# Optimization experiments

Hardware: AMD Instinct MI355X
Metric: run time of the kernel (lower is better)

The kernel has to match this reference:

```python
import jax, jax.numpy as jnp
import numpy as np


def setup_inputs() -> dict:
    key = jax.random.key(0)
    k1, k2, k3 = jax.random.split(key, 3)
    B, L, D = 2, 8192, 1024
    x = jax.random.normal(k1, (B, L, D), dtype=jnp.float32)
    h = jax.random.normal(k2, (L, D), dtype=jnp.float32)
    bias = jax.random.normal(k3, (D,), dtype=jnp.float32) * 0.02
    return {"x": x, "h": h, "bias": bias}


def reference(x, h, bias):
    # x: (B, L, D), h: (filter_len, D), bias: (D,)
    B, L, D = x.shape
    filter_len = h.shape[0]
    # next power of two >= L + filter_len - 1 (static, from shapes)
    fft_size = 1 << int(L + filter_len - 1).bit_length()
    x_f = jnp.fft.rfft(x, n=fft_size, axis=1)          # (B, fft_size//2+1, D) complex
    h_f = jnp.fft.rfft(h, n=fft_size, axis=0)          # (fft_size//2+1, D) complex
    y = jnp.fft.irfft(x_f * h_f[None, :, :], n=fft_size, axis=1)
    y = y[:, :L, :]                                    # causal-length truncation
    return y + bias
```

## Files before the change

### kernel.cpp

```cpp
#include <hip/hip_runtime.h>

#define D_CH   1024
#define L_SEQ  8192
#define TWO_PI 6.28318530717958647692f
#define W_N    3.8349519697141029e-4f
#define W128A  4.90873852123405e-2f

__device__ __forceinline__ unsigned f2bf(float v){
  union { float f; unsigned u; } x; x.f = v;
  unsigned r = x.u + 0x7fffu + ((x.u >> 16) & 1u);
  return r >> 16;
}
__device__ __forceinline__ float bf2f(unsigned v){
  union { float f; unsigned u; } x; x.u = v << 16;
  return x.f;
}
__device__ __forceinline__ unsigned packc(float r, float i){
  return f2bf(r) | (f2bf(i) << 16);
}
__device__ __forceinline__ float2 upk(unsigned u){
  return make_float2(bf2f(u & 0xffffu), bf2f(u >> 16));
}

__device__ __host__ constexpr int bitrev4(int j){
  return ((j&1)<<3)|((j&2)<<1)|((j&4)>>1)|((j&8)>>3);
}
__device__ __host__ constexpr int bitrev3(int j){
  return ((j&1)<<2)|(j&2)|((j&4)>>2);
}

template<int SGN>
__device__ __forceinline__ void dft16(float2* x){
  const float TC[8] = {1.f, 0.9238795325f, 0.7071067812f, 0.3826834324f,
                       0.f, -0.3826834324f, -0.7071067812f, -0.9238795325f};
  const float TS[8] = {0.f, -0.3826834324f, -0.7071067812f, -0.9238795325f,
                       -1.f, -0.9238795325f, -0.7071067812f, -0.3826834324f};
#pragma unroll
  for (int len = 16; len >= 2; len >>= 1){
    const int half = len >> 1, tstep = 16 / len;
#pragma unroll
    for (int st = 0; st < 16; st += len){
#pragma unroll
      for (int j = 0; j < half; j++){
        const float wr = TC[j*tstep];
        const float wi = (SGN > 0) ? TS[j*tstep] : -TS[j*tstep];
        const int a = st + j, b = a + half;
        const float ur = x[a].x, ui = x[a].y;
        const float vr = x[b].x, vi = x[b].y;
        x[a].x = ur + vr; x[a].y = ui + vi;
        const float dr = ur - vr, di = ui - vi;
        x[b].x = dr*wr - di*wi;
        x[b].y = dr*wi + di*wr;
      }
    }
  }
}

template<int SGN>
__device__ __forceinline__ void dft8(float2* x){
  const float TC[4] = {1.f, 0.7071067812f, 0.f, -0.7071067812f};
  const float TS[4] = {0.f, -0.7071067812f, -1.f, -0.7071067812f};
#pragma unroll
  for (int len = 8; len >= 2; len >>= 1){
    const int half = len >> 1, tstep = 8 / len;
#pragma unroll
    for (int st = 0; st < 8; st += len){
#pragma unroll
      for (int j = 0; j < half; j++){
        const float wr = TC[j*tstep];
        const float wi = (SGN > 0) ? TS[j*tstep] : -TS[j*tstep];
        const int a = st + j, b = a + half;
        const float ur = x[a].x, ui = x[a].y;
        const float vr = x[b].x, vi = x[b].y;
        x[a].x = ur + vr; x[a].y = ui + vi;
        const float dr = ur - vr, di = ui - vi;
        x[b].x = dr*wr - di*wi;
        x[b].y = dr*wi + di*wr;
      }
    }
  }
}

template<int SGN>
__device__ __forceinline__ void fft128(float2* v, float2* lds, int lane, int p){
  dft16<SGN>(v);
#pragma unroll
  for (int slot = 0; slot < 16; slot++){
    const int s = bitrev4(slot);
    float sn, cs;
    __sincosf(-(float)SGN * W128A * (float)(p*s), &sn, &cs);
    const float2 a = v[slot];
    lds[(p*16 + s)*64 + lane] = make_float2(a.x*cs - a.y*sn, a.x*sn + a.y*cs);
  }
  __syncthreads();
  float2 t8[8];
#pragma unroll
  for (int c = 0; c < 2; c++){
#pragma unroll
    for (int pp = 0; pp < 8; pp++)
      t8[pp] = lds[(pp*16 + 2*p + c)*64 + lane];
    dft8<SGN>(t8);
#pragma unroll
    for (int t = 0; t < 8; t++) v[c*8 + t] = t8[t];
  }
}

__global__ __launch_bounds__(512, 4)
void k1_step1(const float* __restrict__ x, const float* __restrict__ h,
              unsigned* __restrict__ Az, unsigned* __restrict__ Ah){
  __shared__ float2 lds[8192];
  const int n2 = blockIdx.x, dg = blockIdx.y, mode = blockIdx.z;
  const int lane = threadIdx.x & 63, p = threadIdx.x >> 6;
  const int d = dg*64 + lane;

  float2 v[16];
  if (mode == 0){
    const float* x0 = x;
    const float* x1 = x + (size_t)L_SEQ * D_CH;
#pragma unroll
    for (int q = 0; q < 8; q++){
      const size_t off = (size_t)(n2 + 128*(p + 8*q)) * D_CH + d;
      v[q] = make_float2(x0[off], x1[off]);
    }
  } else {
#pragma unroll
    for (int q = 0; q < 8; q++){
      const size_t off = (size_t)(n2 + 128*(p + 8*q)) * D_CH + d;
      v[q] = make_float2(h[off], 0.0f);
    }
  }
#pragma unroll
  for (int q = 8; q < 16; q++) v[q] = make_float2(0.f, 0.f);

  fft128<1>(v, lds, lane, p);

  unsigned* __restrict__ A = mode ? Ah : Az;
#pragma unroll
  for (int c = 0; c < 2; c++){
#pragma unroll
    for (int t = 0; t < 8; t++){
      const int k1v = (2*p + c) + 16*bitrev3(t);
      float sn, cs;
      __sincosf(-W_N * (float)(k1v * n2), &sn, &cs);
      const float2 a = v[c*8 + t];
      A[((size_t)k1v*128 + n2)*D_CH + d] =
        packc(a.x*cs - a.y*sn, a.x*sn + a.y*cs);
    }
  }
}

__global__ __launch_bounds__(512, 4)
void k2_h(unsigned* __restrict__ Ah){
  __shared__ float2 lds[8192];
  const int k1 = blockIdx.x, dg = blockIdx.y;
  const int lane = threadIdx.x & 63, p = threadIdx.x >> 6;
  const int d = dg*64 + lane;
  const size_t base = (size_t)k1 * 128 * D_CH + d;

  unsigned raw[16];
#pragma unroll
  for (int q = 0; q < 16; q++)
    raw[q] = Ah[base + (size_t)(p + 8*q) * D_CH];
  float2 v[16];
#pragma unroll
  for (int q = 0; q < 16; q++) v[q] = upk(raw[q]);

  fft128<1>(v, lds, lane, p);

#pragma unroll
  for (int c = 0; c < 2; c++){
#pragma unroll
    for (int t = 0; t < 8; t++){
      const int k2 = (2*p + c) + 16*bitrev3(t);
      const float2 a = v[c*8 + t];
      Ah[base + (size_t)k2 * D_CH] = packc(a.x, a.y);
    }
  }
}

__global__ __launch_bounds__(512, 4)
void k2_z(unsigned* __restrict__ Az, const unsigned* __restrict__ Hs){
  __shared__ float2 lds[8192];
  const int k1 = blockIdx.x, dg = blockIdx.y;
  const int lane = threadIdx.x & 63, p = threadIdx.x >> 6;
  const int d = dg*64 + lane;
  const size_t base = (size_t)k1 * 128 * D_CH + d;

  unsigned za[16], ha[16];
#pragma unroll
  for (int q = 0; q < 16; q++)
    za[q] = Az[base + (size_t)(p + 8*q) * D_CH];
#pragma unroll
  for (int c = 0; c < 2; c++){
#pragma unroll
    for (int t = 0; t < 8; t++){
      const int k2 = (2*p + c) + 16*bitrev3(t);
      ha[c*8 + t] = Hs[base + (size_t)k2 * D_CH];
    }
  }

  float2 v[16];
#pragma unroll
  for (int q = 0; q < 16; q++) v[q] = upk(za[q]);

  fft128<1>(v, lds, lane, p);

  const float sc = 1.0f / 16384.0f;
#pragma unroll
  for (int i = 0; i < 16; i++){
    const float2 hsv = upk(ha[i]);
    const float zr = v[i].x, zi = v[i].y;
    v[i] = make_float2((zr*hsv.x - zi*hsv.y) * sc,
                       (zr*hsv.y + zi*hsv.x) * sc);
  }

  __syncthreads();
#pragma unroll
  for (int c = 0; c < 2; c++){
#pragma unroll
    for (int t = 0; t < 8; t++){
      const int k2 = (2*p + c) + 16*bitrev3(t);
      lds[k2*64 + lane] = v[c*8 + t];
    }
  }
  __syncthreads();
#pragma unroll
  for (int q = 0; q < 16; q++) v[q] = lds[(p + 8*q)*64 + lane];
  __syncthreads();

  fft128<-1>(v, lds, lane, p);

#pragma unroll
  for (int c = 0; c < 2; c++){
#pragma unroll
    for (int t = 0; t < 8; t++){
      const int m2 = (2*p + c) + 16*bitrev3(t);
      const float2 a = v[c*8 + t];
      Az[base + (size_t)m2 * D_CH] = packc(a.x, a.y);
    }
  }
}

__global__ __launch_bounds__(512, 4)
void k3_inv2(const unsigned* __restrict__ Bz, const float* __restrict__ bias,
             float* __restrict__ out){
  __shared__ float2 lds[8192];
  const int m2 = blockIdx.x, dg = blockIdx.y;
  const int lane = threadIdx.x & 63, p = threadIdx.x >> 6;
  const int d = dg*64 + lane;
  const float bv = bias[d];

  unsigned raw[16];
#pragma unroll
  for (int q = 0; q < 16; q++){
    const int k1 = p + 8*q;
    raw[q] = Bz[((size_t)k1*128 + m2) * D_CH + d];
  }
  float2 v[16];
#pragma unroll
  for (int q = 0; q < 16; q++){
    const int k1 = p + 8*q;
    float sn, cs;
    __sincosf(W_N * (float)(m2 * k1), &sn, &cs);
    const float2 a = upk(raw[q]);
    v[q] = make_float2(a.x*cs - a.y*sn, a.x*sn + a.y*cs);
  }

  fft128<-1>(v, lds, lane, p);

#pragma unroll
  for (int c = 0; c < 2; c++){
#pragma unroll
    for (int t = 0; t < 8; t += 2){
      const int m1 = (2*p + c) + 16*bitrev3(t);
      const int tseq = m2 + 128*m1;
      const float2 a = v[c*8 + t];
      out[(size_t)tseq * D_CH + d]            = a.x + bv;
      out[(size_t)(L_SEQ + tseq) * D_CH + d]  = a.y + bv;
    }
  }
}

extern "C" void kernel_launch(void* const* d_in, const int* in_sizes, int n_in,
                              void* d_out, int out_size, void* d_ws, size_t ws_size,
                              hipStream_t stream){
  (void)in_sizes; (void)n_in; (void)out_size;
  const float* x    = (const float*)d_in[0];
  const float* h    = (const float*)d_in[1];
  const float* bias = (const float*)d_in[2];
  float* out = (float*)d_out;

  const size_t REGION = (size_t)128 * 128 * D_CH * sizeof(unsigned);
  unsigned *r1, *r2;
  if (ws_size >= 2 * REGION){
    r1 = (unsigned*)d_ws;
    r2 = (unsigned*)((char*)d_ws + REGION);
  } else {
    r1 = (unsigned*)d_out;
    r2 = (unsigned*)d_ws;
  }

  const dim3 blk(512, 1, 1);
  hipLaunchKernelGGL(k1_step1, dim3(128,16,2), blk, 0, stream, x, h, r1, r2);
  hipLaunchKernelGGL(k2_h,     dim3(128,16,1), blk, 0, stream, r2);
  hipLaunchKernelGGL(k2_z,     dim3(128,16,1), blk, 0, stream, r1, r2);
  hipLaunchKernelGGL(k3_inv2,  dim3(128,16,1), blk, 0, stream, r1, bias, out);
}
```

Before: 261.0 us.

## Fuse filter FFT into convolution kernel and halve LDS via two-pass transpose

Merges the separate h-spectrum kernel into the z kernel, so the filter's second-stage FFT is recomputed per block and kept in registers. This removes one launch and a bf16 write and read of the h workspace. The 128-point FFT's LDS transpose is split into two half-size passes, halving shared memory per block, and launch bounds are raised so more blocks can be resident. The cost is extra barriers and a duplicate FFT inside the fused kernel, plus register pressure from the higher occupancy targets.

```diff
diff --git a/kernel.cpp b/kernel.cpp
--- a/kernel.cpp
+++ b/kernel.cpp
@@ -2,7 +2,6 @@
 
 #define D_CH   1024
 #define L_SEQ  8192
-#define TWO_PI 6.28318530717958647692f
 #define W_N    3.8349519697141029e-4f
 #define W128A  4.90873852123405e-2f
 
@@ -85,30 +84,41 @@
 __device__ __forceinline__ void fft128(float2* v, float2* lds, int lane, int p){
   dft16<SGN>(v);
 #pragma unroll
-  for (int slot = 0; slot < 16; slot++){
-    const int s = bitrev4(slot);
+  for (int slot = 0; slot < 8; slot++){
+    const int r = bitrev3(slot);
     float sn, cs;
-    __sincosf(-(float)SGN * W128A * (float)(p*s), &sn, &cs);
+    __sincosf(-(float)SGN * W128A * (float)(p*(2*r)), &sn, &cs);
     const float2 a = v[slot];
-    lds[(p*16 + s)*64 + lane] = make_float2(a.x*cs - a.y*sn, a.x*sn + a.y*cs);
+    lds[(p*8 + r)*64 + lane] = make_float2(a.x*cs - a.y*sn, a.x*sn + a.y*cs);
   }
   __syncthreads();
   float2 t8[8];
 #pragma unroll
-  for (int c = 0; c < 2; c++){
-#pragma unroll
-    for (int pp = 0; pp < 8; pp++)
-      t8[pp] = lds[(pp*16 + 2*p + c)*64 + lane];
-    dft8<SGN>(t8);
-#pragma unroll
-    for (int t = 0; t < 8; t++) v[c*8 + t] = t8[t];
-  }
-}
-
-__global__ __launch_bounds__(512, 4)
+  for (int pp = 0; pp < 8; pp++) t8[pp] = lds[(pp*8 + p)*64 + lane];
+  dft8<SGN>(t8);
+#pragma unroll
+  for (int t = 0; t < 8; t++) v[t] = t8[t];
+  __syncthreads();
+#pragma unroll
+  for (int slot = 8; slot < 16; slot++){
+    const int r = bitrev3(slot - 8);
+    float sn, cs;
+    __sincosf(-(float)SGN * W128A * (float)(p*(2*r+1)), &sn, &cs);
+    const float2 a = v[slot];
+    lds[(p*8 + r)*64 + lane] = make_float2(a.x*cs - a.y*sn, a.x*sn + a.y*cs);
+  }
+  __syncthreads();
+#pragma unroll
+  for (int pp = 0; pp < 8; pp++) t8[pp] = lds[(pp*8 + p)*64 + lane];
+  dft8<SGN>(t8);
+#pragma unroll
+  for (int t = 0; t < 8; t++) v[8 + t] = t8[t];
+}
+
+__global__ __launch_bounds__(512, 8)
 void k1_step1(const float* __restrict__ x, const float* __restrict__ h,
               unsigned* __restrict__ Az, unsigned* __restrict__ Ah){
-  __shared__ float2 lds[8192];
+  __shared__ float2 lds[4096];
   const int n2 = blockIdx.x, dg = blockIdx.y, mode = blockIdx.z;
   const int lane = threadIdx.x & 63, p = threadIdx.x >> 6;
   const int d = dg*64 + lane;
@@ -150,83 +160,68 @@
 }
 
 __global__ __launch_bounds__(512, 4)
-void k2_h(unsigned* __restrict__ Ah){
-  __shared__ float2 lds[8192];
+void k2_zh(unsigned* __restrict__ Az, const unsigned* __restrict__ Ah){
+  __shared__ float2 lds[4096];
   const int k1 = blockIdx.x, dg = blockIdx.y;
   const int lane = threadIdx.x & 63, p = threadIdx.x >> 6;
   const int d = dg*64 + lane;
   const size_t base = (size_t)k1 * 128 * D_CH + d;
 
-  unsigned raw[16];
+  unsigned ha[16], za[16];
 #pragma unroll
   for (int q = 0; q < 16; q++)
-    raw[q] = Ah[base + (size_t)(p + 8*q) * D_CH];
-  float2 v[16];
-#pragma unroll
-  for (int q = 0; q < 16; q++) v[q] = upk(raw[q]);
-
-  fft128<1>(v, lds, lane, p);
-
-#pragma unroll
-  for (int c = 0; c < 2; c++){
-#pragma unroll
-    for (int t = 0; t < 8; t++){
-      const int k2 = (2*p + c) + 16*bitrev3(t);
-      const float2 a = v[c*8 + t];
-      Ah[base + (size_t)k2 * D_CH] = packc(a.x, a.y);
-    }
-  }
-}
-
-__global__ __launch_bounds__(512, 4)
-void k2_z(unsigned* __restrict__ Az, const unsigned* __restrict__ Hs){
-  __shared__ float2 lds[8192];
-  const int k1 = blockIdx.x, dg = blockIdx.y;
-  const int lane = threadIdx.x & 63, p = threadIdx.x >> 6;
-  const int d = dg*64 + lane;
-  const size_t base = (size_t)k1 * 128 * D_CH + d;
-
-  unsigned za[16], ha[16];
+    ha[q] = Ah[base + (size_t)(p + 8*q) * D_CH];
 #pragma unroll
   for (int q = 0; q < 16; q++)
     za[q] = Az[base + (size_t)(p + 8*q) * D_CH];
-#pragma unroll
-  for (int c = 0; c < 2; c++){
-#pragma unroll
-    for (int t = 0; t < 8; t++){
-      const int k2 = (2*p + c) + 16*bitrev3(t);
-      ha[c*8 + t] = Hs[base + (size_t)k2 * D_CH];
-    }
-  }
 
   float2 v[16];
 #pragma unroll
+  for (int q = 0; q < 16; q++) v[q] = upk(ha[q]);
+  fft128<1>(v, lds, lane, p);
+  unsigned hs[16];
+  const float sc = 1.0f / 16384.0f;
+#pragma unroll
+  for (int i = 0; i < 16; i++) hs[i] = packc(v[i].x * sc, v[i].y * sc);
+  __syncthreads();
+
+#pragma unroll
   for (int q = 0; q < 16; q++) v[q] = upk(za[q]);
-
   fft128<1>(v, lds, lane, p);
 
-  const float sc = 1.0f / 16384.0f;
 #pragma unroll
   for (int i = 0; i < 16; i++){
-    const float2 hsv = upk(ha[i]);
+    const float2 hv = upk(hs[i]);
     const float zr = v[i].x, zi = v[i].y;
-    v[i] = make_float2((zr*hsv.x - zi*hsv.y) * sc,
-                       (zr*hsv.y + zi*hsv.x) * sc);
-  }
-
-  __syncthreads();
-#pragma unroll
-  for (int c = 0; c < 2; c++){
-#pragma unroll
-    for (int t = 0; t < 8; t++){
+    v[i] = make_float2(zr*hv.x - zi*hv.y, zr*hv.y + zi*hv.x);
+  }
+
+  __syncthreads();
+  float2 w[16];
+#pragma unroll
+  for (int c = 0; c < 2; c++)
+#pragma unroll
+    for (int t = 0; t < 8; t += 2){
       const int k2 = (2*p + c) + 16*bitrev3(t);
       lds[k2*64 + lane] = v[c*8 + t];
     }
-  }
-  __syncthreads();
-#pragma unroll
-  for (int q = 0; q < 16; q++) v[q] = lds[(p + 8*q)*64 + lane];
-  __syncthreads();
+  __syncthreads();
+#pragma unroll
+  for (int q = 0; q < 8; q++) w[q] = lds[(p + 8*q)*64 + lane];
+  __syncthreads();
+#pragma unroll
+  for (int c = 0; c < 2; c++)
+#pragma unroll
+    for (int t = 1; t < 8; t += 2){
+      const int k2 = (2*p + c) + 16*bitrev3(t) - 64;
+      lds[k2*64 + lane] = v[c*8 + t];
+    }
+  __syncthreads();
+#pragma unroll
+  for (int q = 0; q < 8; q++) w[8 + q] = lds[(p + 8*q)*64 + lane];
+  __syncthreads();
+#pragma unroll
+  for (int q = 0; q < 16; q++) v[q] = w[q];
 
   fft128<-1>(v, lds, lane, p);
 
@@ -241,10 +236,10 @@
   }
 }
 
-__global__ __launch_bounds__(512, 4)
+__global__ __launch_bounds__(512, 6)
 void k3_inv2(const unsigned* __restrict__ Bz, const float* __restrict__ bias,
              float* __restrict__ out){
-  __shared__ float2 lds[8192];
+  __shared__ float2 lds[4096];
   const int m2 = blockIdx.x, dg = blockIdx.y;
   const int lane = threadIdx.x & 63, p = threadIdx.x >> 6;
   const int d = dg*64 + lane;
@@ -302,7 +297,6 @@
 
   const dim3 blk(512, 1, 1);
   hipLaunchKernelGGL(k1_step1, dim3(128,16,2), blk, 0, stream, x, h, r1, r2);
-  hipLaunchKernelGGL(k2_h,     dim3(128,16,1), blk, 0, stream, r2);
-  hipLaunchKernelGGL(k2_z,     dim3(128,16,1), blk, 0, stream, r1, r2);
+  hipLaunchKernelGGL(k2_zh,    dim3(128,16,1), blk, 0, stream, r1, r2);
   hipLaunchKernelGGL(k3_inv2,  dim3(128,16,1), blk, 0, stream, r1, bias, out);
 }
```

Measured after the change: 245.3 us. 1.06x faster.
